# Kernel optimization log

Measured on AMD Instinct MI355X. Metric: run time of the kernel, lower is better.

## Reference

```python
import jax, jax.numpy as jnp
import numpy as np

H = 28; W = 28; N = H * W
P = N              # padded max persistence pairs per homology dimension
T = 32             # landscape resolution
K1, K2 = 2, 3      # K_max for the two topo layers
M0_1, M0_2 = 0.05, 0.2
LIMS = ((1.0, 28.0), (1.0, 28.0))


def _make_nbrs(h, w, conn8):
    idx = np.arange(h * w).reshape(h, w)
    offs = [(-1, 0), (1, 0), (0, -1), (0, 1)]
    if conn8:
        offs += [(-1, -1), (-1, 1), (1, -1), (1, 1)]
    nbrs = []
    for i in range(h):
        for j in range(w):
            cur = [idx[i + a, j + b] for a, b in offs if 0 <= i + a < h and 0 <= j + b < w]
            nbrs.append(np.asarray(cur, np.int64))
    return nbrs

_NBR4 = _make_nbrs(H, W, False)
_NBR8 = _make_nbrs(H, W, True)


def _h0_pairs(vals, nbrs):
    # 0-dim persistence pairs of a vertex-valued sublevel filtration (union-find, elder rule)
    order = np.argsort(vals, kind="stable")
    pos = np.empty(N, np.int64); pos[order] = np.arange(N)
    parent = np.arange(N); birth = np.arange(N)
    added = np.zeros(N, bool)
    bi = np.zeros(P, np.int32); di = np.zeros(P, np.int32)
    k = 0
    def find(x):
        r = x
        while parent[r] != r: r = parent[r]
        while parent[x] != r: parent[x], x = r, parent[x]
        return r
    for v in order:
        added[v] = True
        for u in nbrs[v]:
            if not added[u]: continue
            ru, rv = find(u), find(v)
            if ru == rv: continue
            if pos[birth[ru]] <= pos[birth[rv]]:
                lb = birth[rv]; parent[rv] = ru
            else:
                lb = birth[ru]; parent[ru] = rv
            if k < P:
                bi[k] = lb; di[k] = v; k += 1
    return bi, di


def _pers_pairs_np(x):
    # x: [M, N] -> (birth_idx, death_idx) each [M, 2, P]; padded pairs point at idx 0 (zero persistence)
    x = np.asarray(x, np.float64)
    M = x.shape[0]
    bi = np.zeros((M, 2, P), np.int32); di = np.zeros((M, 2, P), np.int32)
    for m in range(M):
        b0, d0 = _h0_pairs(x[m], _NBR4)      # H0: sublevel, 4-connectivity
        b1, d1 = _h0_pairs(-x[m], _NBR8)     # H1 by Alexander duality: H0 of superlevel, 8-connectivity
        bi[m, 0], di[m, 0] = b0, d0
        bi[m, 1], di[m, 1] = d1, b1          # H1 birth = vals[d1], death = vals[b1]
    return bi, di


def _grid_d2():
    xs = np.linspace(LIMS[0][0], LIMS[0][1], H)
    ys = np.linspace(LIMS[1][0], LIMS[1][1], W)
    gx, gy = np.meshgrid(xs, ys, indexing="ij")
    pts = np.stack([gx.ravel(), gy.ravel()], 1)              # [N, 2] grid coordinates
    d2 = ((pts[:, None, :] - pts[None, :, :]) ** 2).sum(-1)  # [N, N] squared distances
    si = np.argsort(d2, axis=1, kind="stable")
    return jnp.asarray(si), jnp.asarray(np.take_along_axis(d2, si, 1), jnp.float32)

_SORT_IDX, _D2S = _grid_d2()


def dtm(x_flat, m0):
    # weighted distance-to-measure on the pixel grid, r=2; x_flat: [M, N] positive weights
    bound = m0 * jnp.sum(x_flat, -1, keepdims=True)                        # [M, 1]
    ws = x_flat[:, _SORT_IDX]                                              # [M, N, N] weights in distance order
    cum = jnp.cumsum(ws, -1)
    eff = jnp.minimum(jnp.maximum(bound[..., None] - (cum - ws), 0.0), ws) # effective mass per neighbor
    return jnp.sqrt(jnp.sum(eff * _D2S, -1) / bound)                       # [M, N]


def _landscape(vals, bi, di, start, end, K):
    # persistence landscape lambda_k sampled on T points from (birth, death) critical-vertex indices
    M = vals.shape[0]
    mi = jnp.arange(M)[:, None, None]
    b = vals[mi, bi]; d = vals[mi, di]                                     # [M, 2, P]
    t = jnp.linspace(start, end, T, dtype=vals.dtype)                      # [T]
    tent = jnp.maximum(jnp.minimum(t - b[..., None], d[..., None] - t), 0.0)  # [M, 2, P, T]
    lam, _ = jax.lax.top_k(jnp.swapaxes(tent, -1, -2), K)                  # [M, 2, T, K]
    return jnp.swapaxes(lam, -1, -2).reshape(M, 2 * K * T)                 # [M, dims*K*T]


def pl_features(vals, start, end, K):
    M = vals.shape[0]
    bi, di = jax.pure_callback(
        _pers_pairs_np,
        (jax.ShapeDtypeStruct((M, 2, P), np.int32),
         jax.ShapeDtypeStruct((M, 2, P), np.int32)),
        jax.lax.stop_gradient(vals))
    return _landscape(vals, bi, di, start, end, K)


def setup_inputs():
    key = jax.random.key(0)
    ks = jax.random.split(key, 7)
    B = 64
    return {
        "input": jax.random.uniform(ks[0], (B, 1, H, W), jnp.float32, 1e-3, 1.0),
        "w_g1": 0.1 * jax.random.normal(ks[1], (32, 2 * K1 * T), jnp.float32),
        "b_g1": 0.1 * jax.random.normal(ks[2], (32,), jnp.float32),
        "w_g2": 0.1 * jax.random.normal(ks[3], (32, 2 * K2 * T), jnp.float32),
        "b_g2": 0.1 * jax.random.normal(ks[4], (32,), jnp.float32),
        "w_fc": 0.1 * jax.random.normal(ks[5], (10, 64), jnp.float32),
        "b_fc": 0.1 * jax.random.normal(ks[6], (10,), jnp.float32),
    }


def reference(input, w_g1, b_g1, w_g2, b_g2, w_fc, b_fc):
    x_flat = input.reshape(-1, N)                                        # num_channels = 1
    f1 = dtm(x_flat, M0_1)
    f2 = dtm(x_flat, M0_2)
    x1 = jax.nn.relu(pl_features(f1, 0.0, 7.0, K1) @ w_g1.T + b_g1)      # topo layer 1 (start=0, end=7, K=2)
    x2 = jax.nn.relu(pl_features(f2, 1.0, 8.0, K2) @ w_g2.T + b_g2)      # topo layer 2 (start=1, end=8, K=3)
    return jnp.concatenate([x1, x2], -1) @ w_fc.T + b_fc                 # [B, num_classes]
```

## Files before the change

### kernel.cpp

```cpp
#include <hip/hip_runtime.h>

#define HW 28
#define NPIX 784
#define NIMG 64
#define MAXD2 1459
#define MAXREC 5504

#define DXPK 41048u
#define DYPK 34949u

__global__ void consts_sums_kernel(unsigned int* __restrict__ TPK,
                                   const float* __restrict__ x,
                                   float* __restrict__ sums,
                                   float* __restrict__ xT) {
    int tid = threadIdx.x;
    if (blockIdx.x >= NPIX) {
        int m = blockIdx.x - NPIX;
        const float* xr = x + m * NPIX;
        float acc = 0.f;
        for (int j = tid; j < NPIX; j += 256) {
            float v = xr[j];
            xT[j * NIMG + m] = v;
            acc += v;
        }
        for (int off = 32; off > 0; off >>= 1) acc += __shfl_down(acc, off, 64);
        __shared__ float red[4];
        int lane = tid & 63, w = tid >> 6;
        if (lane == 0) red[w] = acc;
        __syncthreads();
        if (tid == 0) sums[m] = red[0] + red[1] + red[2] + red[3];
        return;
    }
    __shared__ int cnt[MAXD2];
    __shared__ int d2v[NPIX];
    __shared__ int wtot[4];
    int i = blockIdx.x;
    for (int b = tid; b < MAXD2; b += 256) cnt[b] = 0;
    __syncthreads();
    int ii = i / HW, ij = i % HW;
    for (int j = tid; j < NPIX; j += 256) {
        int di = ii - j / HW, dj = ij - j % HW;
        int d = di * di + dj * dj;
        d2v[j] = d;
        atomicAdd(&cnt[d], 1);
    }
    __syncthreads();
    int b0 = tid * 6;
    int lc[6];
    int s0 = 0;
    #pragma unroll
    for (int t = 0; t < 6; ++t) {
        int b = b0 + t;
        lc[t] = (b < MAXD2) ? cnt[b] : 0;
        s0 += lc[t];
    }
    int lane = tid & 63, wv = tid >> 6;
    int v = s0;
    for (int off = 1; off < 64; off <<= 1) {
        int t2 = __shfl_up(v, off, 64);
        if (lane >= off) v += t2;
    }
    if (lane == 63) wtot[wv] = v;
    __syncthreads();
    int wadd = 0;
    for (int w2 = 0; w2 < wv; ++w2) wadd += wtot[w2];
    int run = wadd + v - s0;
    __syncthreads();
    #pragma unroll
    for (int t = 0; t < 6; ++t) {
        int b = b0 + t;
        if (b < MAXD2) { cnt[b] = run; run += lc[t]; }
    }
    __syncthreads();
    for (int j = tid; j < NPIX; j += 256) {
        int d = d2v[j];
        int slot = atomicAdd(&cnt[d], 1);
        TPK[i * NPIX + slot] = (unsigned)j | ((unsigned)d << 16);
    }
}

__global__ void __launch_bounds__(64) dtm_kernel(const unsigned int* __restrict__ TPK,
                                                 const float* __restrict__ xT,
                                                 const float* __restrict__ sums,
                                                 float* __restrict__ F) {
    int lane = threadIdx.x;
    int i = blockIdx.x;
    float s = sums[lane];
    float bound1 = 0.05f * s, bound2 = 0.2f * s;
    const unsigned int* tp = TPK + (size_t)i * NPIX;
    float cum = 0.f, acc1 = 0.f, acc2 = 0.f;
    for (int t0 = 0; t0 < NPIX; t0 += 8) {
        unsigned int e[8];
        #pragma unroll
        for (int u = 0; u < 8; ++u) e[u] = tp[t0 + u];
        float w[8];
        #pragma unroll
        for (int u = 0; u < 8; ++u) w[u] = xT[(e[u] & 0xffffu) * NIMG + lane];
        #pragma unroll
        for (int u = 0; u < 8; ++u) {
            float d2 = (float)(e[u] >> 16);
            float ce = cum;
            cum += w[u];
            acc1 += fminf(fmaxf(bound1 - ce, 0.f), w[u]) * d2;
            acc2 += fminf(fmaxf(bound2 - ce, 0.f), w[u]) * d2;
        }
        if (__ballot(cum < bound2) == 0ull) break;
    }
    F[0 * NIMG * NPIX + lane * NPIX + i] = sqrtf(acc1 / bound1);
    F[1 * NIMG * NPIX + lane * NPIX + i] = sqrtf(acc2 / bound2);
}

template<int NN>
__device__ int uf_basin_run(const int* posA, const int* ordA,
                            int* bas, unsigned int* pb, int* comp,
                            int* recs, int* pairsI,
                            int2* mergeLDS, int* shInts, int* wtot16) {
    const int tid = threadIdx.x;
    const int lane = tid & 63, wv = tid >> 6;

    for (int s = tid; s < NPIX; s += 1024) {
        int si = s / HW, sj = s % HW;
        int bestPos = posA[s], best = s;
        #pragma unroll
        for (int o = 0; o < NN; ++o) {
            int dx = ((DXPK >> (2 * o)) & 3) - 1;
            int dy = ((DYPK >> (2 * o)) & 3) - 1;
            int ui = si + dx, uj = sj + dy;
            if ((unsigned)ui < (unsigned)HW && (unsigned)uj < (unsigned)HW) {
                int u = ui * HW + uj;
                int pu = posA[u];
                if (pu < bestPos) { bestPos = pu; best = u; }
            }
        }
        bas[s] = best;
    }
    __syncthreads();

    for (int it = 0; it < 10; ++it) {
        int changed = 0;
        for (int s = tid; s < NPIX; s += 1024) {
            int b = bas[s];
            int bb = bas[b];
            if (bb != b) { bas[s] = bb; changed = 1; }
        }
        if (__syncthreads_count(changed) == 0) break;
    }

    for (int s = tid; s < NPIX; s += 1024)
        pb[s] = ((unsigned)posA[s] << 10) | (unsigned)bas[s];
    __syncthreads();

    int nrec = 0;
    {
        int r = tid;
        int cnt = 0;
        int myr[NN - 1];
        int got[NN - 1];
        #pragma unroll
        for (int t = 0; t < NN - 1; ++t) { got[t] = -1; myr[t] = 0; }
        if (r > 0 && r < NPIX) {
            int v = ordA[r];
            int vi = v / HW, vj = v % HW;
            int pivot = (int)(pb[v] & 1023u);
            #pragma unroll
            for (int o = 0; o < NN; ++o) {
                int dx = ((DXPK >> (2 * o)) & 3) - 1;
                int dy = ((DYPK >> (2 * o)) & 3) - 1;
                int ui = vi + dx, uj = vj + dy;
                if ((unsigned)ui < (unsigned)HW && (unsigned)uj < (unsigned)HW) {
                    int u = ui * HW + uj;
                    unsigned e = pb[u];
                    if ((int)(e >> 10) < r) {
                        int b = (int)(e & 1023u);
                        bool dup = (b == pivot);
                        #pragma unroll
                        for (int t = 0; t < NN - 1; ++t) dup = dup || (got[t] == b);
                        if (!dup) {
                            #pragma unroll
                            for (int t = 0; t < NN - 1; ++t)
                                if (t == cnt) { got[t] = b; myr[t] = (v << 20) | (pivot << 10) | b; }
                            cnt++;
                        }
                    }
                }
            }
        }
        int p = cnt;
        for (int off = 1; off < 64; off <<= 1) {
            int t2 = __shfl_up(p, off, 64);
            if (lane >= off) p += t2;
        }
        if (lane == 63) wtot16[wv] = p;
        __syncthreads();
        int wadd = 0;
        for (int w2 = 0; w2 < wv; ++w2) wadd += wtot16[w2];
        int tot = 0;
        #pragma unroll
        for (int w2 = 0; w2 < 16; ++w2) tot += wtot16[w2];
        int excl = wadd + p - cnt;
        #pragma unroll
        for (int t = 0; t < NN - 1; ++t)
            if (t < cnt) recs[excl + t] = myr[t];
        nrec = tot;
        __syncthreads();
    }

    int k = 0;
    for (int base = 0; base < nrec; base += 64) {
        int nrem = 0;
        if (wv == 0) {
            int idx = base + lane;
            int rec = (idx < nrec) ? recs[idx] : 0;
            int pa = (rec >> 10) & 1023, pbn = rec & 1023;
            int ka = 0, kb = 0;
            if (idx < nrec) { ka = comp[pa]; kb = comp[pbn]; }
            for (;;) {
                unsigned long long d = __ballot(ka != kb);
                if (d == 0ull) break;
                int i = (int)__ffsll((long long)d) - 1;
                int sA = __builtin_amdgcn_readlane(ka, i);
                int sB = __builtin_amdgcn_readlane(kb, i);
                int w = min(sA, sB), l = max(sA, sB);
                int sv = __builtin_amdgcn_readlane(rec, i) >> 20;
                if (lane == 0) {
                    pairsI[k] = (l & 1023) | (sv << 10);
                    mergeLDS[nrem] = make_int2(l, w);
                }
                k++;
                ka = (ka == l) ? w : ka;
                kb = (kb == l) ? w : kb;
                nrem++;
                if (nrem == 63) {
                    for (int s = lane; s < NPIX; s += 64) {
                        int cv = comp[s], c0 = cv;
                        for (int e = 0; e < nrem; ++e) {
                            int2 me = mergeLDS[e];
                            cv = (cv == me.x) ? me.y : cv;
                        }
                        if (cv != c0) comp[s] = cv;
                    }
                    if (idx < nrec) { ka = comp[pa]; kb = comp[pbn]; }
                    nrem = 0;
                }
            }
            if (lane == 0) shInts[0] = nrem;
        }
        __syncthreads();
        int nr = shInts[0];
        if (nr > 0) {
            for (int s = tid; s < NPIX; s += 1024) {
                int cv = comp[s], c0 = cv;
                for (int e = 0; e < nr; ++e) {
                    int2 me = mergeLDS[e];
                    cv = (cv == me.x) ? me.y : cv;
                }
                if (cv != c0) comp[s] = cv;
            }
        }
        __syncthreads();
    }
    if (tid == 0) shInts[1] = k;
    __syncthreads();
    return shInts[1];
}

__global__ void __launch_bounds__(1024) uf_land_kernel(const float* __restrict__ F,
                                                       float* __restrict__ LAM1,
                                                       float* __restrict__ LAM2) {
    __shared__ int posA[NPIX], ordA[NPIX], bas[NPIX], comp[NPIX], pairsI[NPIX];
    __shared__ unsigned int pbArr[NPIX];
    __shared__ alignas(16) unsigned long long key64[NPIX];
    __shared__ float fv[NPIX];
    __shared__ int recs[MAXREC];
    __shared__ int2 mergeLDS[64];
    __shared__ int shInts[2];
    __shared__ int wtot16[16];
    int tid = threadIdx.x;
    int task = blockIdx.x;
    int feat = task >> 7;
    int dir = (task >> 6) & 1;
    int m = task & 63;
    const float* fr = F + feat * NIMG * NPIX + m * NPIX;

    for (int j = tid; j < NPIX; j += 1024) {
        float f = fr[j];
        fv[j] = f;
        unsigned int b = __float_as_uint(f);
        if (dir) b = ~b;
        key64[j] = ((unsigned long long)b << 10) | (unsigned)j;
    }
    __syncthreads();

    if (tid < 256) {
        unsigned long long pki[4];
        int rank[4] = {0, 0, 0, 0};
        bool val[4];
        #pragma unroll
        for (int r = 0; r < 4; ++r) {
            int i = tid + 256 * r;
            val[r] = (i < NPIX);
            pki[r] = val[r] ? key64[i] : 0ull;
        }
        const ulonglong2* k2 = (const ulonglong2*)key64;
        for (int c = 0; c < NPIX / 2; ++c) {
            ulonglong2 kv = k2[c];
            #pragma unroll
            for (int r = 0; r < 4; ++r)
                rank[r] += (int)(kv.x < pki[r]) + (int)(kv.y < pki[r]);
        }
        #pragma unroll
        for (int r = 0; r < 4; ++r) {
            if (val[r]) {
                int i = tid + 256 * r;
                posA[i] = rank[r];
                ordA[rank[r]] = i;
            }
        }
    }
    __syncthreads();
    for (int s = tid; s < NPIX; s += 1024) comp[s] = (posA[s] << 10) | s;

    int k;
    if (dir == 0) k = uf_basin_run<4>(posA, ordA, bas, pbArr, comp, recs, pairsI,
                                      mergeLDS, shInts, wtot16);
    else          k = uf_basin_run<8>(posA, ordA, bas, pbArr, comp, recs, pairsI,
                                      mergeLDS, shInts, wtot16);

    if (tid < 32) {
        int t = tid;
        float start = (feat == 0) ? 0.f : 1.f;
        float end   = (feat == 0) ? 7.f : 8.f;
        float tv = start + (end - start) * ((float)t / 31.f);
        float v0 = 0.f, v1 = 0.f, v2 = 0.f;
        for (int p = 0; p < k; ++p) {
            int pi = pairsI[p];
            float fb = fv[pi & 1023], fd = fv[pi >> 10];
            float bb = dir ? fd : fb;
            float dd = dir ? fb : fd;
            float tent = fmaxf(fminf(tv - bb, dd - tv), 0.f);
            if (tent > v0)      { v2 = v1; v1 = v0; v0 = tent; }
            else if (tent > v1) { v2 = v1; v1 = tent; }
            else if (tent > v2) { v2 = tent; }
        }
        if (feat == 0) {
            float* lam = LAM1 + m * 128 + dir * 64;
            lam[0 * 32 + t] = v0;
            lam[1 * 32 + t] = v1;
        } else {
            float* lam = LAM2 + m * 192 + dir * 96;
            lam[0 * 32 + t] = v0;
            lam[1 * 32 + t] = v1;
            lam[2 * 32 + t] = v2;
        }
    }
}

__global__ void mlp_kernel(const float* __restrict__ LAM1, const float* __restrict__ LAM2,
                           const float* __restrict__ w1, const float* __restrict__ b1,
                           const float* __restrict__ w2, const float* __restrict__ b2,
                           const float* __restrict__ wf, const float* __restrict__ bf,
                           float* __restrict__ out) {
    __shared__ float xc[64];
    int m = blockIdx.x;
    int n = threadIdx.x;
    if (n < 32) {
        float acc = b1[n];
        const float* l = LAM1 + m * 128;
        for (int c = 0; c < 128; ++c) acc += w1[n * 128 + c] * l[c];
        xc[n] = fmaxf(acc, 0.f);
    } else {
        int n2 = n - 32;
        float acc = b2[n2];
        const float* l = LAM2 + m * 192;
        for (int c = 0; c < 192; ++c) acc += w2[n2 * 192 + c] * l[c];
        xc[n] = fmaxf(acc, 0.f);
    }
    __syncthreads();
    if (n < 10) {
        float acc = bf[n];
        for (int c = 0; c < 64; ++c) acc += wf[n * 64 + c] * xc[c];
        out[m * 10 + n] = acc;
    }
}

extern "C" void kernel_launch(void* const* d_in, const int* in_sizes, int n_in,
                              void* d_out, int out_size, void* d_ws, size_t ws_size,
                              hipStream_t stream) {
    const float* x  = (const float*)d_in[0];
    const float* w1 = (const float*)d_in[1];
    const float* b1 = (const float*)d_in[2];
    const float* w2 = (const float*)d_in[3];
    const float* b2 = (const float*)d_in[4];
    const float* wf = (const float*)d_in[5];
    const float* bf = (const float*)d_in[6];
    float* out = (float*)d_out;

    char* ws = (char*)d_ws;
    size_t off = 0;
    unsigned int* TPK = (unsigned int*)(ws + off); off += (size_t)NPIX * NPIX * 4;
    float* XT   = (float*)(ws + off); off += (size_t)NPIX * NIMG * 4;
    float* SUMS = (float*)(ws + off); off += 256;
    float* F    = (float*)(ws + off); off += (size_t)2 * NIMG * NPIX * 4;
    float* LAM1 = (float*)(ws + off); off += (size_t)NIMG * 128 * 4;
    float* LAM2 = (float*)(ws + off); off += (size_t)NIMG * 192 * 4;

    consts_sums_kernel<<<NPIX + NIMG, 256, 0, stream>>>(TPK, x, SUMS, XT);
    dtm_kernel<<<NPIX, 64, 0, stream>>>(TPK, XT, SUMS, F);
    uf_land_kernel<<<256, 1024, 0, stream>>>(F, LAM1, LAM2);
    mlp_kernel<<<NIMG, 64, 0, stream>>>(LAM1, LAM2, w1, b1, w2, b2, wf, bf, out);
}
```

Baseline: 126.8 us.

## Exploit grid symmetry to build only canonical distance-sorted neighbor tables

```diff
diff --git a/kernel.cpp b/kernel.cpp
--- a/kernel.cpp
+++ b/kernel.cpp
@@ -3,19 +3,20 @@
 #define HW 28
 #define NPIX 784
 #define NIMG 64
+#define NCAN 105
 #define MAXD2 1459
 #define MAXREC 5504
 
 #define DXPK 41048u
 #define DYPK 34949u
 
-__global__ void consts_sums_kernel(unsigned int* __restrict__ TPK,
+__global__ void consts_sums_kernel(unsigned int* __restrict__ TPKC,
                                    const float* __restrict__ x,
                                    float* __restrict__ sums,
                                    float* __restrict__ xT) {
     int tid = threadIdx.x;
-    if (blockIdx.x >= NPIX) {
-        int m = blockIdx.x - NPIX;
+    if (blockIdx.x >= NCAN) {
+        int m = blockIdx.x - NCAN;
         const float* xr = x + m * NPIX;
         float acc = 0.f;
         for (int j = tid; j < NPIX; j += 256) {
@@ -31,15 +32,18 @@
         if (tid == 0) sums[m] = red[0] + red[1] + red[2] + red[3];
         return;
     }
+    int bi = blockIdx.x;
+    int a = 0, rem = bi;
+    while (rem >= 14 - a) { rem -= 14 - a; a++; }
+    int b = a + rem;
+
     __shared__ int cnt[MAXD2];
     __shared__ int d2v[NPIX];
     __shared__ int wtot[4];
-    int i = blockIdx.x;
-    for (int b = tid; b < MAXD2; b += 256) cnt[b] = 0;
-    __syncthreads();
-    int ii = i / HW, ij = i % HW;
+    for (int bb = tid; bb < MAXD2; bb += 256) cnt[bb] = 0;
+    __syncthreads();
     for (int j = tid; j < NPIX; j += 256) {
-        int di = ii - j / HW, dj = ij - j % HW;
+        int di = a - j / HW, dj = b - j % HW;
         int d = di * di + dj * dj;
         d2v[j] = d;
         atomicAdd(&cnt[d], 1);
@@ -50,8 +54,8 @@
     int s0 = 0;
     #pragma unroll
     for (int t = 0; t < 6; ++t) {
-        int b = b0 + t;
-        lc[t] = (b < MAXD2) ? cnt[b] : 0;
+        int bb = b0 + t;
+        lc[t] = (bb < MAXD2) ? cnt[bb] : 0;
         s0 += lc[t];
     }
     int lane = tid & 63, wv = tid >> 6;
@@ -68,41 +72,57 @@
     __syncthreads();
     #pragma unroll
     for (int t = 0; t < 6; ++t) {
-        int b = b0 + t;
-        if (b < MAXD2) { cnt[b] = run; run += lc[t]; }
+        int bb = b0 + t;
+        if (bb < MAXD2) { cnt[bb] = run; run += lc[t]; }
     }
     __syncthreads();
     for (int j = tid; j < NPIX; j += 256) {
         int d = d2v[j];
         int slot = atomicAdd(&cnt[d], 1);
-        TPK[i * NPIX + slot] = (unsigned)j | ((unsigned)d << 16);
-    }
-}
-
-__global__ void __launch_bounds__(64) dtm_kernel(const unsigned int* __restrict__ TPK,
+        TPKC[bi * NPIX + slot] =
+            (unsigned)((j / HW) << 5) | (unsigned)(j % HW) | ((unsigned)d << 16);
+    }
+}
+
+__global__ void __launch_bounds__(64) dtm_kernel(const unsigned int* __restrict__ TPKC,
                                                  const float* __restrict__ xT,
                                                  const float* __restrict__ sums,
                                                  float* __restrict__ F) {
     int lane = threadIdx.x;
     int i = blockIdx.x;
+    int r = i / HW, c = i % HW;
+    int fa = (r > 13), fb = (c > 13);
+    int a = fa ? 27 - r : r;
+    int b = fb ? 27 - c : c;
+    int sw = (a > b);
+    if (sw) { int t = a; a = b; b = t; }
+    int cidx = a * 14 - (a * (a - 1)) / 2 + (b - a);
+    const unsigned int* tp = TPKC + (size_t)cidx * NPIX;
+
     float s = sums[lane];
     float bound1 = 0.05f * s, bound2 = 0.2f * s;
-    const unsigned int* tp = TPK + (size_t)i * NPIX;
     float cum = 0.f, acc1 = 0.f, acc2 = 0.f;
     for (int t0 = 0; t0 < NPIX; t0 += 8) {
-        unsigned int e[8];
-        #pragma unroll
-        for (int u = 0; u < 8; ++u) e[u] = tp[t0 + u];
+        int j[8]; float d2[8];
+        #pragma unroll
+        for (int u = 0; u < 8; ++u) {
+            unsigned e = tp[t0 + u];
+            int rj = (int)((e >> 5) & 31u), cj = (int)(e & 31u);
+            int rr = sw ? cj : rj, cc = sw ? rj : cj;
+            if (fa) rr = 27 - rr;
+            if (fb) cc = 27 - cc;
+            j[u] = rr * HW + cc;
+            d2[u] = (float)(e >> 16);
+        }
         float w[8];
         #pragma unroll
-        for (int u = 0; u < 8; ++u) w[u] = xT[(e[u] & 0xffffu) * NIMG + lane];
+        for (int u = 0; u < 8; ++u) w[u] = xT[j[u] * NIMG + lane];
         #pragma unroll
         for (int u = 0; u < 8; ++u) {
-            float d2 = (float)(e[u] >> 16);
             float ce = cum;
             cum += w[u];
-            acc1 += fminf(fmaxf(bound1 - ce, 0.f), w[u]) * d2;
-            acc2 += fminf(fmaxf(bound2 - ce, 0.f), w[u]) * d2;
+            acc1 += fminf(fmaxf(bound1 - ce, 0.f), w[u]) * d2[u];
+            acc2 += fminf(fmaxf(bound2 - ce, 0.f), w[u]) * d2[u];
         }
         if (__ballot(cum < bound2) == 0ull) break;
     }
@@ -397,15 +417,15 @@
 
     char* ws = (char*)d_ws;
     size_t off = 0;
-    unsigned int* TPK = (unsigned int*)(ws + off); off += (size_t)NPIX * NPIX * 4;
+    unsigned int* TPKC = (unsigned int*)(ws + off); off += (size_t)NCAN * NPIX * 4;
     float* XT   = (float*)(ws + off); off += (size_t)NPIX * NIMG * 4;
     float* SUMS = (float*)(ws + off); off += 256;
     float* F    = (float*)(ws + off); off += (size_t)2 * NIMG * NPIX * 4;
     float* LAM1 = (float*)(ws + off); off += (size_t)NIMG * 128 * 4;
     float* LAM2 = (float*)(ws + off); off += (size_t)NIMG * 192 * 4;
 
-    consts_sums_kernel<<<NPIX + NIMG, 256, 0, stream>>>(TPK, x, SUMS, XT);
-    dtm_kernel<<<NPIX, 64, 0, stream>>>(TPK, XT, SUMS, F);
+    consts_sums_kernel<<<NCAN + NIMG, 256, 0, stream>>>(TPKC, x, SUMS, XT);
+    dtm_kernel<<<NPIX, 64, 0, stream>>>(TPKC, XT, SUMS, F);
     uf_land_kernel<<<256, 1024, 0, stream>>>(F, LAM1, LAM2);
     mlp_kernel<<<NIMG, 64, 0, stream>>>(LAM1, LAM2, w1, b1, w2, b2, wf, bf, out);
 }
```

New measurement: 127.4 us. About the same (+0.4%).
